# Performance work log

Measured on AMD Instinct MI355X. Metric: run time of the kernel, lower is better.

## Reference

```python
import jax, jax.numpy as jnp
import numpy as np
import math

B, S, D = 4, 1024, 1024
H, DK = 16, 64
NUM_BUCKETS = 32
MAX_DISTANCE = 128


def _relative_position_bucket(relative_position, bidirectional=True,
                              num_buckets=32, max_distance=128):
    # faithful port of T5's bucketing
    relative_buckets = jnp.zeros_like(relative_position)
    if bidirectional:
        num_buckets //= 2
        relative_buckets = relative_buckets + (relative_position > 0).astype(jnp.int32) * num_buckets
        relative_position = jnp.abs(relative_position)
    else:
        relative_position = -jnp.minimum(relative_position, jnp.zeros_like(relative_position))
    max_exact = num_buckets // 2
    is_small = relative_position < max_exact
    rp_safe = jnp.maximum(relative_position, 1)  # avoid log(0); masked by is_small
    rel_if_large = max_exact + (
        jnp.log(rp_safe.astype(jnp.float32) / max_exact)
        / math.log(max_distance / max_exact) * (num_buckets - max_exact)
    ).astype(jnp.int32)
    rel_if_large = jnp.minimum(rel_if_large, num_buckets - 1)
    return relative_buckets + jnp.where(is_small, relative_position, rel_if_large)


def compute_bias(rel_bias_emb, query_length, key_length):
    ctx = jnp.arange(query_length, dtype=jnp.int32)[:, None]
    mem = jnp.arange(key_length, dtype=jnp.int32)[None, :]
    rp = mem - ctx  # [q, k]
    buckets = _relative_position_bucket(rp, bidirectional=True,
                                        num_buckets=NUM_BUCKETS,
                                        max_distance=MAX_DISTANCE)
    values = rel_bias_emb[buckets]          # [q, k, h]
    return jnp.transpose(values, (2, 0, 1))[None]  # [1, h, q, k]


def setup_inputs() -> dict:
    key = jax.random.key(0)
    ks = jax.random.split(key, 6)
    s = 1.0 / math.sqrt(D)
    return {
        "hidden_states": jax.random.normal(ks[0], (B, S, D), jnp.float32),
        "Wq": jax.random.normal(ks[1], (D, H * DK), jnp.float32) * s,
        "Wk": jax.random.normal(ks[2], (D, H * DK), jnp.float32) * s,
        "Wv": jax.random.normal(ks[3], (D, H * DK), jnp.float32) * s,
        "Wo": jax.random.normal(ks[4], (H * DK, D), jnp.float32) * s,
        "rel_bias_emb": jax.random.normal(ks[5], (NUM_BUCKETS, H), jnp.float32),
    }


def reference(hidden_states, Wq, Wk, Wv, Wo, rel_bias_emb):
    b, s, _ = hidden_states.shape

    def shape_heads(x):  # [b, s, h*dk] -> [b, h, s, dk]
        return x.reshape(b, s, H, DK).transpose(0, 2, 1, 3)

    q = shape_heads(hidden_states @ Wq)
    k = shape_heads(hidden_states @ Wk)
    v = shape_heads(hidden_states @ Wv)

    # T5 attention: no 1/sqrt(dk) scaling
    scores = jnp.einsum('bhqd,bhkd->bhqk', q, k)
    position_bias = compute_bias(rel_bias_emb, s, s)  # [1, h, s, s]
    scores = scores + position_bias
    attn = jax.nn.softmax(scores.astype(jnp.float32), axis=-1).astype(scores.dtype)
    ctx = jnp.einsum('bhqk,bhkd->bhqd', attn, v)
    ctx = ctx.transpose(0, 2, 1, 3).reshape(b, s, H * DK)
    return ctx @ Wo
```

## Files before the change

kernel.cpp:

```cpp
#include <hip/hip_runtime.h>

typedef unsigned short u16;
typedef unsigned int u32;
typedef __bf16 bf16x8 __attribute__((ext_vector_type(8)));
typedef float f32x4 __attribute__((ext_vector_type(4)));

#define MFMA16(a, b, c) __builtin_amdgcn_mfma_f32_16x16x32_bf16(a, b, c, 0, 0, 0)
#define LOG2E 1.4426950408889634f

__device__ __forceinline__ u16 f2bf(float f) {
  u32 u = __float_as_uint(f);
  u += 0x7FFFu + ((u >> 16) & 1u);
  return (u16)(u >> 16);
}

__device__ __forceinline__ void gld16(u16* lds, const u16* g) {
  __builtin_amdgcn_global_load_lds((const __attribute__((address_space(1))) void*)g,
                                   (__attribute__((address_space(3))) void*)lds,
                                   16, 0, 0);
}

__device__ __forceinline__ int t5_bucket(int rp) {
  int ret = rp > 0 ? 16 : 0;
  int a = rp < 0 ? -rp : rp;
  int b;
  if      (a <  8) b = a;
  else if (a < 12) b = 8;
  else if (a < 16) b = 9;
  else if (a < 23) b = 10;
  else if (a < 32) b = 11;
  else if (a < 46) b = 12;
  else if (a < 64) b = 13;
  else if (a < 91) b = 14;
  else             b = 15;
  return ret + b;
}

__global__ __launch_bounds__(256) void prep(const float4* __restrict__ X, ushort4* __restrict__ Xb,
                                            const float* __restrict__ w0, const float* __restrict__ w1,
                                            const float* __restrict__ w2, const float* __restrict__ w3,
                                            u16* __restrict__ out) {
  int bid = blockIdx.x;
  if (bid < 512) {
#pragma unroll
    for (int i = 0; i < 8; i++) {
      int g = bid * 2048 + i * 256 + threadIdx.x;
      float4 v = X[g];
      ushort4 o;
      o.x = f2bf(v.x); o.y = f2bf(v.y); o.z = f2bf(v.z); o.w = f2bf(v.w);
      Xb[g] = o;
    }
    return;
  }
  bid -= 512;
  __shared__ __align__(16) u16 tb[64 * 68];
  const int col = threadIdx.x & 63;
  const int rowo = threadIdx.x >> 6;
#pragma unroll 1
  for (int t2 = 0; t2 < 2; t2++) {
    const int tile = bid * 2 + t2;
    const int z = tile >> 8, t = tile & 255;
    const float* W = (z == 0) ? w0 : (z == 1) ? w1 : (z == 2) ? w2 : w3;
    u16* O = out + z * 1048576;
    const int n0 = (t & 15) * 64, k0 = (t >> 4) * 64;
#pragma unroll
    for (int r = 0; r < 16; r++) {
      int kl = r * 4 + rowo;
      tb[col * 68 + kl] = f2bf(W[(k0 + kl) * 1024 + n0 + col]);
    }
    __syncthreads();
#pragma unroll
    for (int r = 0; r < 16; r++) {
      int nl = r * 4 + rowo;
      O[(n0 + nl) * 1024 + k0 + col] = tb[nl * 68 + col];
    }
    __syncthreads();
  }
}

__global__ __launch_bounds__(256) void gemm128(const u16* __restrict__ A,
                                               const u16* __restrict__ BtBase,
                                               u16* __restrict__ outp) {
  __shared__ __align__(16) u16 smem[18432];
  u16* sA = smem;
  u16* sB = smem + 8192;
  const int tid = threadIdx.x, lane = tid & 63, wave = tid >> 6;
  const int l15 = lane & 15, quad = lane >> 4;
  const int wm = (wave >> 1) * 64, wn = (wave & 1) * 64;

  const int id = blockIdx.x + blockIdx.y * 24;
  const int xcd = id & 7, jj = id >> 3;
  const int nz = (jj % 12) + (xcd & 1) * 12;
  const int ymb = (jj / 12) + (xcd >> 1) * 8;
  const int n = nz / 3, z = nz % 3;
  const int m0 = ymb * 128, n0 = n * 128;
  const u16* Bt = BtBase + z * 1048576;

  f32x4 acc[4][4];
  const f32x4 vz = {0.f, 0.f, 0.f, 0.f};
#pragma unroll
  for (int i = 0; i < 4; i++)
#pragma unroll
    for (int j = 0; j < 4; j++) acc[i][j] = vz;

  const int sx = l15 & 7;

  for (int kt = 0; kt < 16; kt++) {
    const int ka = kt * 64;
#pragma unroll
    for (int r = 0; r < 4; r++) {
      int cb = r * 256 + wave * 64;
      int cc = cb + lane;
      int row = cc >> 3, c8 = (cc & 7) ^ (row & 7);
      gld16(sA + cb * 8, A  + (m0 + row) * 1024 + ka + c8 * 8);
      gld16(sB + cb * 8, Bt + (n0 + row) * 1024 + ka + c8 * 8);
    }
    __syncthreads();
#pragma unroll
    for (int kk = 0; kk < 2; kk++) {
      bf16x8 af[4], bg[4];
      int g8 = kk * 4 + quad;
#pragma unroll
      for (int mt = 0; mt < 4; mt++)
        af[mt] = *(const bf16x8*)(sA + (wm + mt * 16 + l15) * 64 + (g8 ^ sx) * 8);
#pragma unroll
      for (int nt = 0; nt < 4; nt++)
        bg[nt] = *(const bf16x8*)(sB + (wn + nt * 16 + l15) * 64 + (g8 ^ sx) * 8);
#pragma unroll
      for (int mt = 0; mt < 4; mt++)
#pragma unroll
        for (int nt = 0; nt < 4; nt++)
          acc[mt][nt] = MFMA16(af[mt], bg[nt], acc[mt][nt]);
    }
    __syncthreads();
  }

  if (z == 2) {
    u16* O = outp + z * 4194304;
#pragma unroll
    for (int mt = 0; mt < 4; mt++)
#pragma unroll
      for (int nt = 0; nt < 4; nt++) {
        int col = wn + nt * 16 + l15;
        int rowb = wm + mt * 16 + quad * 4;
        uint2 p;
        p.x = (u32)f2bf(acc[mt][nt][0]) | ((u32)f2bf(acc[mt][nt][1]) << 16);
        p.y = (u32)f2bf(acc[mt][nt][2]) | ((u32)f2bf(acc[mt][nt][3]) << 16);
        *(uint2*)(smem + col * 136 + rowb) = p;
      }
    __syncthreads();
    const int b = m0 >> 10, sbase = m0 & 1023;
#pragma unroll
    for (int p = 0; p < 8; p++) {
      int g = p * 256 + tid;
      int col = g >> 4, chunk = g & 15;
      uint4 v = *(const uint4*)(smem + col * 136 + chunk * 8);
      int nn = n0 + col, hh = nn >> 6, dk = nn & 63;
      *(uint4*)(O + ((b * 16 + hh) * 64 + dk) * 1024 + sbase + chunk * 8) = v;
    }
  } else {
    u16* O = outp + z * 4194304;
    const float scl = (z == 0) ? LOG2E : 1.0f;
#pragma unroll
    for (int mt = 0; mt < 4; mt++)
#pragma unroll
      for (int nt = 0; nt < 4; nt++) {
        int rowb = wm + mt * 16 + quad * 4;
        int colb = wn + nt * 16 + l15;
#pragma unroll
        for (int reg = 0; reg < 4; reg++)
          smem[(rowb + reg) * 144 + colb] = f2bf(acc[mt][nt][reg] * scl);
      }
    __syncthreads();
    const int b = m0 >> 10, sbase = m0 & 1023;
#pragma unroll
    for (int p = 0; p < 8; p++) {
      int g = p * 256 + tid;
      int ml = g >> 4, c = g & 15;
      uint4 v = *(const uint4*)(smem + ml * 144 + c * 8);
      int nn = n0 + c * 8, hh = nn >> 6, dk = nn & 63;
      *(uint4*)(O + (b * 16 + hh) * 65536 + (sbase + ml) * 64 + dk) = v;
    }
  }
}

__global__ __launch_bounds__(256) void attn(const u16* __restrict__ Q, const u16* __restrict__ K,
                                            const u16* __restrict__ V, const float* __restrict__ emb,
                                            u16* __restrict__ ctx) {
  __shared__ __align__(16) u16 sK[64 * 64];
  __shared__ __align__(16) u16 sV[64 * 64];
  __shared__ __align__(16) u16 sP[128 * 72];
  __shared__ __align__(16) float4 bt4[1156];
  const int tid = threadIdx.x, lane = tid & 63, wave = tid >> 6;
  const int l15 = lane & 15, quad = lane >> 4;
  const int bh = blockIdx.x, qt = blockIdx.y;
  const int h = bh & 15, b = bh >> 4;
  const u16* Qp = Q + bh * 65536 + qt * 8192;
  const u16* Kp = K + bh * 65536;
  const u16* Vp = V + bh * 65536;
  const int sx = l15 & 7;

  bf16x8 aq[2][2];
#pragma unroll
  for (int u = 0; u < 2; u++)
#pragma unroll
    for (int kk = 0; kk < 2; kk++)
      aq[u][kk] = *(const bf16x8*)(Qp + (wave * 32 + u * 16 + l15) * 64 + kk * 32 + quad * 8);

  for (int i = tid; i < 1156; i += 256) {
    int rp0 = i - 127 - qt * 128;
    float4 v;
    v.x = emb[t5_bucket(rp0)     * 16 + h] * LOG2E;
    v.y = emb[t5_bucket(rp0 + 1) * 16 + h] * LOG2E;
    v.z = emb[t5_bucket(rp0 + 2) * 16 + h] * LOG2E;
    v.w = emb[t5_bucket(rp0 + 3) * 16 + h] * LOG2E;
    bt4[i] = v;
  }
  const float bias_pos = emb[31 * 16 + h] * LOG2E;
  const float bias_neg = emb[15 * 16 + h] * LOG2E;

  float2 ls2[2] = {{0.f, 0.f}, {0.f, 0.f}};
  f32x4 oc[2][4];
  const f32x4 vzero = {0.f, 0.f, 0.f, 0.f};
#pragma unroll
  for (int u = 0; u < 2; u++)
#pragma unroll
    for (int nt = 0; nt < 4; nt++) oc[u][nt] = vzero;

  __syncthreads();

#pragma unroll 1
  for (int j = 0; j < 16; j++) {
    const u16* Kj = Kp + j * 4096;
#pragma unroll
    for (int r = 0; r < 2; r++) {
      int cb = r * 256 + wave * 64;
      int cc = cb + lane;
      int row = cc >> 3, c8 = (cc & 7) ^ (row & 7);
      gld16(sK + cb * 8, Kj + row * 64 + c8 * 8);
      gld16(sV + cb * 8, Vp + row * 1024 + j * 64 + c8 * 8);
    }
    __syncthreads();

    f32x4 sc[4][2];
    const int rp_min = j * 64 - qt * 128 - 127;
    const int rp_max = j * 64 + 63 - qt * 128;
    if (rp_min >= 91) {
#pragma unroll
      for (int mt = 0; mt < 4; mt++)
#pragma unroll
        for (int u = 0; u < 2; u++) { sc[mt][u][0] = bias_pos; sc[mt][u][1] = bias_pos; sc[mt][u][2] = bias_pos; sc[mt][u][3] = bias_pos; }
    } else if (rp_max <= -91) {
#pragma unroll
      for (int mt = 0; mt < 4; mt++)
#pragma unroll
        for (int u = 0; u < 2; u++) { sc[mt][u][0] = bias_neg; sc[mt][u][1] = bias_neg; sc[mt][u][2] = bias_neg; sc[mt][u][3] = bias_neg; }
    } else {
#pragma unroll
      for (int mt = 0; mt < 4; mt++)
#pragma unroll
        for (int u = 0; u < 2; u++) {
          int idx = j * 64 + mt * 16 + quad * 4 - wave * 32 - u * 16 - l15 + 127;
          float4 bv4 = bt4[idx];
          sc[mt][u][0] = bv4.x; sc[mt][u][1] = bv4.y; sc[mt][u][2] = bv4.z; sc[mt][u][3] = bv4.w;
        }
    }
#pragma unroll
    for (int kk = 0; kk < 2; kk++) {
      bf16x8 ak[4];
      int g8 = kk * 4 + quad;
#pragma unroll
      for (int mt = 0; mt < 4; mt++)
        ak[mt] = *(const bf16x8*)(sK + (mt * 16 + l15) * 64 + (g8 ^ sx) * 8);
#pragma unroll
      for (int mt = 0; mt < 4; mt++)
#pragma unroll
        for (int u = 0; u < 2; u++)
          sc[mt][u] = MFMA16(ak[mt], aq[u][kk], sc[mt][u]);
    }

#pragma unroll
    for (int u = 0; u < 2; u++) {
      const int prow = wave * 32 + u * 16 + l15;
#pragma unroll
      for (int mt = 0; mt < 4; mt++) {
        u32 b0 = __float_as_uint(__builtin_amdgcn_exp2f(sc[mt][u][0]));
        u32 b1 = __float_as_uint(__builtin_amdgcn_exp2f(sc[mt][u][1]));
        u32 b2 = __float_as_uint(__builtin_amdgcn_exp2f(sc[mt][u][2]));
        u32 b3 = __float_as_uint(__builtin_amdgcn_exp2f(sc[mt][u][3]));
        u32 t0 = b0 & 0xFFFF0000u, t1 = b1 & 0xFFFF0000u;
        u32 t2 = b2 & 0xFFFF0000u, t3 = b3 & 0xFFFF0000u;
        ls2[u].x += __uint_as_float(t0) + __uint_as_float(t2);
        ls2[u].y += __uint_as_float(t1) + __uint_as_float(t3);
        uint2 pk;
        pk.x = (t0 >> 16) | t1;
        pk.y = (t2 >> 16) | t3;
        *(uint2*)(sP + prow * 72 + mt * 16 + quad * 4) = pk;
      }
    }
    asm volatile("s_waitcnt lgkmcnt(0)" ::: "memory");

#pragma unroll
    for (int kk = 0; kk < 2; kk++) {
      bf16x8 ap[2];
      int g8 = kk * 4 + quad;
#pragma unroll
      for (int u = 0; u < 2; u++)
        ap[u] = *(const bf16x8*)(sP + (wave * 32 + u * 16 + l15) * 72 + kk * 32 + quad * 8);
#pragma unroll
      for (int nt = 0; nt < 4; nt++) {
        bf16x8 bv = *(const bf16x8*)(sV + (nt * 16 + l15) * 64 + (g8 ^ sx) * 8);
#pragma unroll
        for (int u = 0; u < 2; u++)
          oc[u][nt] = MFMA16(ap[u], bv, oc[u][nt]);
      }
    }
    __syncthreads();
  }

  float lsum[2];
#pragma unroll
  for (int u = 0; u < 2; u++) {
    lsum[u] = ls2[u].x + ls2[u].y;
    lsum[u] += __shfl_xor(lsum[u], 16, 64);
    lsum[u] += __shfl_xor(lsum[u], 32, 64);
  }
  float linv[2][4];
#pragma unroll
  for (int u = 0; u < 2; u++)
#pragma unroll
    for (int reg = 0; reg < 4; reg++)
      linv[u][reg] = __builtin_amdgcn_rcpf(__shfl(lsum[u], quad * 4 + reg, 64));

  u16* cb2 = ctx + b * 1048576 + (qt * 128 + wave * 32) * 1024 + h * 64;
#pragma unroll
  for (int u = 0; u < 2; u++)
#pragma unroll
    for (int nt = 0; nt < 4; nt++)
#pragma unroll
      for (int reg = 0; reg < 4; reg++)
        cb2[(u * 16 + quad * 4 + reg) * 1024 + nt * 16 + l15] = f2bf(oc[u][nt][reg] * linv[u][reg]);
}

__global__ __launch_bounds__(256) void gemm_o(const u16* __restrict__ A,
                                              const u16* __restrict__ Bt,
                                              float* __restrict__ O) {
  __shared__ __align__(16) u16 sA[128 * 64];
  __shared__ __align__(16) u16 sB[64 * 64];
  const int tid = threadIdx.x, lane = tid & 63, wave = tid >> 6;
  const int l15 = lane & 15, quad = lane >> 4;
  const int wm = (wave >> 1) * 64, wn = (wave & 1) * 32;
  const int m0 = blockIdx.x * 128, n0 = blockIdx.y * 64;

  f32x4 acc[4][2];
  const f32x4 vz = {0.f, 0.f, 0.f, 0.f};
#pragma unroll
  for (int i = 0; i < 4; i++) { acc[i][0] = vz; acc[i][1] = vz; }

  const int sx = l15 & 7;

  for (int kt = 0; kt < 16; kt++) {
    const int ka = kt * 64;
#pragma unroll
    for (int r = 0; r < 4; r++) {
      int cb = r * 256 + wave * 64;
      int cc = cb + lane;
      int row = cc >> 3, c8 = (cc & 7) ^ (row & 7);
      gld16(sA + cb * 8, A + (m0 + row) * 1024 + ka + c8 * 8);
    }
#pragma unroll
    for (int r = 0; r < 2; r++) {
      int cb = r * 256 + wave * 64;
      int cc = cb + lane;
      int row = cc >> 3, c8 = (cc & 7) ^ (row & 7);
      gld16(sB + cb * 8, Bt + (n0 + row) * 1024 + ka + c8 * 8);
    }
    __syncthreads();
#pragma unroll
    for (int kk = 0; kk < 2; kk++) {
      bf16x8 af[4], bg[2];
      int g8 = kk * 4 + quad;
#pragma unroll
      for (int mt = 0; mt < 4; mt++)
        af[mt] = *(const bf16x8*)(sA + (wm + mt * 16 + l15) * 64 + (g8 ^ sx) * 8);
#pragma unroll
      for (int nt = 0; nt < 2; nt++)
        bg[nt] = *(const bf16x8*)(sB + (wn + nt * 16 + l15) * 64 + (g8 ^ sx) * 8);
#pragma unroll
      for (int mt = 0; mt < 4; mt++)
#pragma unroll
        for (int nt = 0; nt < 2; nt++)
          acc[mt][nt] = MFMA16(af[mt], bg[nt], acc[mt][nt]);
    }
    __syncthreads();
  }

#pragma unroll
  for (int mt = 0; mt < 4; mt++)
#pragma unroll
    for (int nt = 0; nt < 2; nt++)
#pragma unroll
      for (int reg = 0; reg < 4; reg++) {
        int row = m0 + wm + mt * 16 + quad * 4 + reg;
        int col = n0 + wn + nt * 16 + l15;
        O[row * 1024 + col] = acc[mt][nt][reg];
      }
}

extern "C" void kernel_launch(void* const* d_in, const int* in_sizes, int n_in,
                              void* d_out, int out_size, void* d_ws, size_t ws_size,
                              hipStream_t stream) {
  (void)in_sizes; (void)n_in; (void)out_size; (void)ws_size;
  const float* X   = (const float*)d_in[0];
  const float* Wq  = (const float*)d_in[1];
  const float* Wk  = (const float*)d_in[2];
  const float* Wv  = (const float*)d_in[3];
  const float* Wo  = (const float*)d_in[4];
  const float* emb = (const float*)d_in[5];

  char* ws = (char*)d_ws;
  u16* Xb  = (u16*)(ws);
  u16* Wt  = (u16*)(ws + (8u  << 20));
  u16* Qb  = (u16*)(ws + (16u << 20));
  u16* Ctx = (u16*)(ws + (40u << 20));

  prep<<<1024, 256, 0, stream>>>((const float4*)X, (ushort4*)Xb, Wq, Wk, Wv, Wo, Wt);
  gemm128<<<dim3(24, 32), 256, 0, stream>>>(Xb, Wt, Qb);
  attn<<<dim3(64, 8), 256, 0, stream>>>(Qb, Qb + 4194304, Qb + 2 * 4194304, emb, Ctx);
  gemm_o<<<dim3(32, 16), 256, 0, stream>>>(Ctx, Wt + 3 * 1048576, (float*)d_out);
}
```

Measured before the change: 173.2 us.

## Register-prefetch next K tile in GEMMs and enlarge output GEMM tile

Both the QKV projection GEMM and the output GEMM drop direct global-to-LDS loads. They now prefetch the next K-slice into registers while the current slice is multiplied, then write it to shared memory after the barrier. The output GEMM tile grows from 128x64 to 128x128, halving the grid and doubling per-wave MFMA work and B-tile reuse, and launch bounds are added to cap register use. The aim is to hide global load latency behind compute. The cost is higher register pressure, extra VGPR-to-LDS store instructions, and fewer blocks for the output GEMM (256 on a large GPU).

New measurement: 293.4 us. 1.69x slower.

```diff
diff --git a/kernel.cpp b/kernel.cpp
--- a/kernel.cpp
+++ b/kernel.cpp
@@ -78,9 +78,9 @@
   }
 }
 
-__global__ __launch_bounds__(256) void gemm128(const u16* __restrict__ A,
-                                               const u16* __restrict__ BtBase,
-                                               u16* __restrict__ outp) {
+__global__ __launch_bounds__(256, 3) void gemm128(const u16* __restrict__ A,
+                                                  const u16* __restrict__ BtBase,
+                                                  u16* __restrict__ outp) {
   __shared__ __align__(16) u16 smem[18432];
   u16* sA = smem;
   u16* sB = smem + 8192;
@@ -94,7 +94,17 @@
   const int ymb = (jj / 12) + (xcd >> 1) * 8;
   const int n = nz / 3, z = nz % 3;
   const int m0 = ymb * 128, n0 = n * 128;
-  const u16* Bt = BtBase + z * 1048576;
+  const u16* Ab = A + m0 * 1024;
+  const u16* Bb = BtBase + z * 1048576 + n0 * 1024;
+
+  int srow[4], soff[4], sdst[4];
+#pragma unroll
+  for (int r = 0; r < 4; r++) {
+    int cc = r * 256 + wave * 64 + lane;
+    srow[r] = cc >> 3;
+    soff[r] = srow[r] * 1024 + ((cc & 7) ^ (srow[r] & 7)) * 8;
+    sdst[r] = cc * 8;
+  }
 
   f32x4 acc[4][4];
   const f32x4 vz = {0.f, 0.f, 0.f, 0.f};
@@ -105,17 +115,29 @@
 
   const int sx = l15 & 7;
 
+  uint4 pa[4], pb[4];
+#pragma unroll
+  for (int r = 0; r < 4; r++) {
+    pa[r] = *(const uint4*)(Ab + soff[r]);
+    pb[r] = *(const uint4*)(Bb + soff[r]);
+  }
+#pragma unroll
+  for (int r = 0; r < 4; r++) {
+    *(uint4*)(sA + sdst[r]) = pa[r];
+    *(uint4*)(sB + sdst[r]) = pb[r];
+  }
+
+#pragma unroll 1
   for (int kt = 0; kt < 16; kt++) {
-    const int ka = kt * 64;
-#pragma unroll
-    for (int r = 0; r < 4; r++) {
-      int cb = r * 256 + wave * 64;
-      int cc = cb + lane;
-      int row = cc >> 3, c8 = (cc & 7) ^ (row & 7);
-      gld16(sA + cb * 8, A  + (m0 + row) * 1024 + ka + c8 * 8);
-      gld16(sB + cb * 8, Bt + (n0 + row) * 1024 + ka + c8 * 8);
-    }
-    __syncthreads();
+    __syncthreads();
+    if (kt < 15) {
+      const int ka = (kt + 1) * 64;
+#pragma unroll
+      for (int r = 0; r < 4; r++) {
+        pa[r] = *(const uint4*)(Ab + ka + soff[r]);
+        pb[r] = *(const uint4*)(Bb + ka + soff[r]);
+      }
+    }
 #pragma unroll
     for (int kk = 0; kk < 2; kk++) {
       bf16x8 af[4], bg[4];
@@ -133,6 +155,13 @@
           acc[mt][nt] = MFMA16(af[mt], bg[nt], acc[mt][nt]);
     }
     __syncthreads();
+    if (kt < 15) {
+#pragma unroll
+      for (int r = 0; r < 4; r++) {
+        *(uint4*)(sA + sdst[r]) = pa[r];
+        *(uint4*)(sB + sdst[r]) = pb[r];
+      }
+    }
   }
 
   if (z == 2) {
@@ -342,63 +371,89 @@
         cb2[(u * 16 + quad * 4 + reg) * 1024 + nt * 16 + l15] = f2bf(oc[u][nt][reg] * linv[u][reg]);
 }
 
-__global__ __launch_bounds__(256) void gemm_o(const u16* __restrict__ A,
-                                              const u16* __restrict__ Bt,
-                                              float* __restrict__ O) {
+__global__ __launch_bounds__(256, 2) void gemm_o(const u16* __restrict__ A,
+                                                 const u16* __restrict__ Bt,
+                                                 float* __restrict__ O) {
   __shared__ __align__(16) u16 sA[128 * 64];
-  __shared__ __align__(16) u16 sB[64 * 64];
+  __shared__ __align__(16) u16 sB[128 * 64];
   const int tid = threadIdx.x, lane = tid & 63, wave = tid >> 6;
   const int l15 = lane & 15, quad = lane >> 4;
-  const int wm = (wave >> 1) * 64, wn = (wave & 1) * 32;
-  const int m0 = blockIdx.x * 128, n0 = blockIdx.y * 64;
-
-  f32x4 acc[4][2];
+  const int wm = (wave >> 1) * 64, wn = (wave & 1) * 64;
+  const int m0 = blockIdx.x * 128, n0 = blockIdx.y * 128;
+  const u16* Ab = A + m0 * 1024;
+  const u16* Bb = Bt + n0 * 1024;
+
+  int srow[4], soff[4], sdst[4];
+#pragma unroll
+  for (int r = 0; r < 4; r++) {
+    int cc = r * 256 + wave * 64 + lane;
+    srow[r] = cc >> 3;
+    soff[r] = srow[r] * 1024 + ((cc & 7) ^ (srow[r] & 7)) * 8;
+    sdst[r] = cc * 8;
+  }
+
+  f32x4 acc[4][4];
   const f32x4 vz = {0.f, 0.f, 0.f, 0.f};
 #pragma unroll
-  for (int i = 0; i < 4; i++) { acc[i][0] = vz; acc[i][1] = vz; }
+  for (int i = 0; i < 4; i++)
+#pragma unroll
+    for (int j = 0; j < 4; j++) acc[i][j] = vz;
 
   const int sx = l15 & 7;
 
+  uint4 pa[4], pb[4];
+#pragma unroll
+  for (int r = 0; r < 4; r++) {
+    pa[r] = *(const uint4*)(Ab + soff[r]);
+    pb[r] = *(const uint4*)(Bb + soff[r]);
+  }
+#pragma unroll
+  for (int r = 0; r < 4; r++) {
+    *(uint4*)(sA + sdst[r]) = pa[r];
+    *(uint4*)(sB + sdst[r]) = pb[r];
+  }
+
+#pragma unroll 1
   for (int kt = 0; kt < 16; kt++) {
-    const int ka = kt * 64;
-#pragma unroll
-    for (int r = 0; r < 4; r++) {
-      int cb = r * 256 + wave * 64;
-      int cc = cb + lane;
-      int row = cc >> 3, c8 = (cc & 7) ^ (row & 7);
-      gld16(sA + cb * 8, A + (m0 + row) * 1024 + ka + c8 * 8);
-    }
-#pragma unroll
-    for (int r = 0; r < 2; r++) {
-      int cb = r * 256 + wave * 64;
-      int cc = cb + lane;
-      int row = cc >> 3, c8 = (cc & 7) ^ (row & 7);
-      gld16(sB + cb * 8, Bt + (n0 + row) * 1024 + ka + c8 * 8);
-    }
-    __syncthreads();
+    __syncthreads();
+    if (kt < 15) {
+      const int ka = (kt + 1) * 64;
+#pragma unroll
+      for (int r = 0; r < 4; r++) {
+        pa[r] = *(const uint4*)(Ab + ka + soff[r]);
+        pb[r] = *(const uint4*)(Bb + ka + soff[r]);
+      }
+    }
 #pragma unroll
     for (int kk = 0; kk < 2; kk++) {
-      bf16x8 af[4], bg[2];
+      bf16x8 af[4], bg[4];
       int g8 = kk * 4 + quad;
 #pragma unroll
       for (int mt = 0; mt < 4; mt++)
         af[mt] = *(const bf16x8*)(sA + (wm + mt * 16 + l15) * 64 + (g8 ^ sx) * 8);
 #pragma unroll
-      for (int nt = 0; nt < 2; nt++)
+      for (int nt = 0; nt < 4; nt++)
         bg[nt] = *(const bf16x8*)(sB + (wn + nt * 16 + l15) * 64 + (g8 ^ sx) * 8);
 #pragma unroll
       for (int mt = 0; mt < 4; mt++)
 #pragma unroll
-        for (int nt = 0; nt < 2; nt++)
+        for (int nt = 0; nt < 4; nt++)
           acc[mt][nt] = MFMA16(af[mt], bg[nt], acc[mt][nt]);
     }
     __syncthreads();
+    if (kt < 15) {
+#pragma unroll
+      for (int r = 0; r < 4; r++) {
+        *(uint4*)(sA + sdst[r]) = pa[r];
+        *(uint4*)(sB + sdst[r]) = pb[r];
+      }
+    }
   }
 
 #pragma unroll
   for (int mt = 0; mt < 4; mt++)
 #pragma unroll
-    for (int nt = 0; nt < 2; nt++)
+    for (int nt = 0; nt < 4; nt++)
 #pragma unroll
       for (int reg = 0; reg < 4; reg++) {
         int row = m0 + wm + mt * 16 + quad * 4 + reg;
@@ -427,5 +482,5 @@
   prep<<<1024, 256, 0, stream>>>((const float4*)X, (ushort4*)Xb, Wq, Wk, Wv, Wo, Wt);
   gemm128<<<dim3(24, 32), 256, 0, stream>>>(Xb, Wt, Qb);
   attn<<<dim3(64, 8), 256, 0, stream>>>(Qb, Qb + 4194304, Qb + 2 * 4194304, emb, Ctx);
-  gemm_o<<<dim3(32, 16), 256, 0, stream>>>(Ctx, Wt + 3 * 1048576, (float*)d_out);
-}
+  gemm_o<<<dim3(32, 8), 256, 0, stream>>>(Ctx, Wt + 3 * 1048576, (float*)d_out);
+}
```

## Double-buffer LDS loads in QKV and output GEMMs with async prefetch

Applied to the files above, without the earlier changes.

Both GEMM kernels now use two LDS buffers. The next k-tile's global_load_lds is issued before computing on the current one, and the waits are manual vmcnt/s_barrier instead of full __syncthreads, so memory latency overlaps with MFMA work. The QKV GEMM switches to 32-wide k-tiles with a new XOR swizzle so the double buffer fits in the same LDS. The output GEMM changes its tile shape to 64x128 with four waves along N, and its grid changes to match. The trade-offs are more LDS per block and a hand-counted vmcnt that must match the number of loads in flight.

Result: faster. 164.8 us (-4.8%).

```diff
diff --git a/kernel.cpp b/kernel.cpp
--- a/kernel.cpp
+++ b/kernel.cpp
@@ -82,8 +82,6 @@
                                                const u16* __restrict__ BtBase,
                                                u16* __restrict__ outp) {
   __shared__ __align__(16) u16 smem[18432];
-  u16* sA = smem;
-  u16* sB = smem + 8192;
   const int tid = threadIdx.x, lane = tid & 63, wave = tid >> 6;
   const int l15 = lane & 15, quad = lane >> 4;
   const int wm = (wave >> 1) * 64, wn = (wave & 1) * 64;
@@ -94,7 +92,13 @@
   const int ymb = (jj / 12) + (xcd >> 1) * 8;
   const int n = nz / 3, z = nz % 3;
   const int m0 = ymb * 128, n0 = n * 128;
-  const u16* Bt = BtBase + z * 1048576;
+  const u16* Ab = A + m0 * 1024;
+  const u16* Bb = BtBase + z * 1048576 + n0 * 1024;
+
+  int cc0 = tid, cc1 = 256 + tid;
+  int row0 = cc0 >> 2, row1 = cc1 >> 2;
+  int aoff0 = row0 * 1024 + (((cc0 & 3) ^ ((row0 >> 1) & 3)) * 8);
+  int aoff1 = row1 * 1024 + (((cc1 & 3) ^ ((row1 >> 1) & 3)) * 8);
 
   f32x4 acc[4][4];
   const f32x4 vz = {0.f, 0.f, 0.f, 0.f};
@@ -103,37 +107,45 @@
 #pragma unroll
     for (int j = 0; j < 4; j++) acc[i][j] = vz;
 
-  const int sx = l15 & 7;
-
-  for (int kt = 0; kt < 16; kt++) {
-    const int ka = kt * 64;
-#pragma unroll
-    for (int r = 0; r < 4; r++) {
-      int cb = r * 256 + wave * 64;
-      int cc = cb + lane;
-      int row = cc >> 3, c8 = (cc & 7) ^ (row & 7);
-      gld16(sA + cb * 8, A  + (m0 + row) * 1024 + ka + c8 * 8);
-      gld16(sB + cb * 8, Bt + (n0 + row) * 1024 + ka + c8 * 8);
-    }
-    __syncthreads();
-#pragma unroll
-    for (int kk = 0; kk < 2; kk++) {
-      bf16x8 af[4], bg[4];
-      int g8 = kk * 4 + quad;
-#pragma unroll
-      for (int mt = 0; mt < 4; mt++)
-        af[mt] = *(const bf16x8*)(sA + (wm + mt * 16 + l15) * 64 + (g8 ^ sx) * 8);
+  const int sk = (l15 >> 1) & 3;
+
+  {
+    u16* st = smem;
+    gld16(st + cc0 * 8, Ab + aoff0);
+    gld16(st + cc1 * 8, Ab + aoff1);
+    gld16(st + 4096 + cc0 * 8, Bb + aoff0);
+    gld16(st + 4096 + cc1 * 8, Bb + aoff1);
+  }
+
+#pragma unroll 1
+  for (int kt = 0; kt < 32; kt++) {
+    u16* st = smem + (kt & 1) * 8192;
+    if (kt < 31) {
+      u16* dst = smem + ((kt + 1) & 1) * 8192;
+      const int ka = (kt + 1) * 32;
+      gld16(dst + cc0 * 8, Ab + ka + aoff0);
+      gld16(dst + cc1 * 8, Ab + ka + aoff1);
+      gld16(dst + 4096 + cc0 * 8, Bb + ka + aoff0);
+      gld16(dst + 4096 + cc1 * 8, Bb + ka + aoff1);
+      asm volatile("s_waitcnt vmcnt(4)\n\ts_barrier" ::: "memory");
+    } else {
+      asm volatile("s_waitcnt vmcnt(0)\n\ts_barrier" ::: "memory");
+    }
+    bf16x8 af[4], bg[4];
+#pragma unroll
+    for (int mt = 0; mt < 4; mt++)
+      af[mt] = *(const bf16x8*)(st + (wm + mt * 16 + l15) * 32 + ((quad ^ sk) * 8));
+#pragma unroll
+    for (int nt = 0; nt < 4; nt++)
+      bg[nt] = *(const bf16x8*)(st + 4096 + (wn + nt * 16 + l15) * 32 + ((quad ^ sk) * 8));
+#pragma unroll
+    for (int mt = 0; mt < 4; mt++)
 #pragma unroll
       for (int nt = 0; nt < 4; nt++)
-        bg[nt] = *(const bf16x8*)(sB + (wn + nt * 16 + l15) * 64 + (g8 ^ sx) * 8);
-#pragma unroll
-      for (int mt = 0; mt < 4; mt++)
-#pragma unroll
-        for (int nt = 0; nt < 4; nt++)
-          acc[mt][nt] = MFMA16(af[mt], bg[nt], acc[mt][nt]);
-    }
-    __syncthreads();
-  }
+        acc[mt][nt] = MFMA16(af[mt], bg[nt], acc[mt][nt]);
+    asm volatile("s_barrier" ::: "memory");
+  }
+  __syncthreads();
 
   if (z == 2) {
     u16* O = outp + z * 4194304;
@@ -345,12 +357,26 @@
 __global__ __launch_bounds__(256) void gemm_o(const u16* __restrict__ A,
                                               const u16* __restrict__ Bt,
                                               float* __restrict__ O) {
-  __shared__ __align__(16) u16 sA[128 * 64];
-  __shared__ __align__(16) u16 sB[64 * 64];
+  __shared__ __align__(16) u16 smem[24576];
   const int tid = threadIdx.x, lane = tid & 63, wave = tid >> 6;
   const int l15 = lane & 15, quad = lane >> 4;
-  const int wm = (wave >> 1) * 64, wn = (wave & 1) * 32;
-  const int m0 = blockIdx.x * 128, n0 = blockIdx.y * 64;
+  const int m0 = blockIdx.x * 64, n0 = blockIdx.y * 128;
+  const u16* Ab = A + m0 * 1024;
+  const u16* Bb = Bt + n0 * 1024;
+  const int wn = wave * 32;
+
+  int ac = tid, bc0 = tid, bc1 = 256 + tid, bc2 = 512 + tid, bc3 = 768 + tid;
+  int ar0 = tid >> 3, ar1 = (256 + tid) >> 3;
+  int aoff0 = ar0 * 1024 + (((tid & 7) ^ (ar0 & 7)) * 8);
+  int aoff1 = ar1 * 1024 + ((((256 + tid) & 7) ^ (ar1 & 7)) * 8);
+  int boff[4], bdst[4];
+#pragma unroll
+  for (int r = 0; r < 4; r++) {
+    int cc = r * 256 + tid;
+    int row = cc >> 3;
+    boff[r] = row * 1024 + (((cc & 7) ^ (row & 7)) * 8);
+    bdst[r] = cc * 8;
+  }
 
   f32x4 acc[4][2];
   const f32x4 vz = {0.f, 0.f, 0.f, 0.f};
@@ -359,40 +385,45 @@
 
   const int sx = l15 & 7;
 
+  {
+    u16* st = smem;
+    gld16(st + tid * 8, Ab + aoff0);
+    gld16(st + (256 + tid) * 8, Ab + aoff1);
+#pragma unroll
+    for (int r = 0; r < 4; r++) gld16(st + 4096 + bdst[r], Bb + boff[r]);
+  }
+
+#pragma unroll 1
   for (int kt = 0; kt < 16; kt++) {
-    const int ka = kt * 64;
-#pragma unroll
-    for (int r = 0; r < 4; r++) {
-      int cb = r * 256 + wave * 64;
-      int cc = cb + lane;
-      int row = cc >> 3, c8 = (cc & 7) ^ (row & 7);
-      gld16(sA + cb * 8, A + (m0 + row) * 1024 + ka + c8 * 8);
-    }
-#pragma unroll
-    for (int r = 0; r < 2; r++) {
-      int cb = r * 256 + wave * 64;
-      int cc = cb + lane;
-      int row = cc >> 3, c8 = (cc & 7) ^ (row & 7);
-      gld16(sB + cb * 8, Bt + (n0 + row) * 1024 + ka + c8 * 8);
-    }
-    __syncthreads();
+    u16* st = smem + (kt & 1) * 12288;
+    if (kt < 15) {
+      u16* dst = smem + ((kt + 1) & 1) * 12288;
+      const int ka = (kt + 1) * 64;
+      gld16(dst + tid * 8, Ab + ka + aoff0);
+      gld16(dst + (256 + tid) * 8, Ab + ka + aoff1);
+#pragma unroll
+      for (int r = 0; r < 4; r++) gld16(dst + 4096 + bdst[r], Bb + ka + boff[r]);
+      asm volatile("s_waitcnt vmcnt(6)\n\ts_barrier" ::: "memory");
+    } else {
+      asm volatile("s_waitcnt vmcnt(0)\n\ts_barrier" ::: "memory");
+    }
 #pragma unroll
     for (int kk = 0; kk < 2; kk++) {
       bf16x8 af[4], bg[2];
       int g8 = kk * 4 + quad;
 #pragma unroll
       for (int mt = 0; mt < 4; mt++)
-        af[mt] = *(const bf16x8*)(sA + (wm + mt * 16 + l15) * 64 + (g8 ^ sx) * 8);
+        af[mt] = *(const bf16x8*)(st + (mt * 16 + l15) * 64 + ((g8 ^ sx) * 8));
 #pragma unroll
       for (int nt = 0; nt < 2; nt++)
-        bg[nt] = *(const bf16x8*)(sB + (wn + nt * 16 + l15) * 64 + (g8 ^ sx) * 8);
+        bg[nt] = *(const bf16x8*)(st + 4096 + (wn + nt * 16 + l15) * 64 + ((g8 ^ sx) * 8));
 #pragma unroll
       for (int mt = 0; mt < 4; mt++)
 #pragma unroll
         for (int nt = 0; nt < 2; nt++)
           acc[mt][nt] = MFMA16(af[mt], bg[nt], acc[mt][nt]);
     }
-    __syncthreads();
+    asm volatile("s_barrier" ::: "memory");
   }
 
 #pragma unroll
@@ -401,7 +432,7 @@
     for (int nt = 0; nt < 2; nt++)
 #pragma unroll
       for (int reg = 0; reg < 4; reg++) {
-        int row = m0 + wm + mt * 16 + quad * 4 + reg;
+        int row = m0 + mt * 16 + quad * 4 + reg;
         int col = n0 + wn + nt * 16 + l15;
         O[row * 1024 + col] = acc[mt][nt][reg];
       }
@@ -427,5 +458,5 @@
   prep<<<1024, 256, 0, stream>>>((const float4*)X, (ushort4*)Xb, Wq, Wk, Wv, Wo, Wt);
   gemm128<<<dim3(24, 32), 256, 0, stream>>>(Xb, Wt, Qb);
   attn<<<dim3(64, 8), 256, 0, stream>>>(Qb, Qb + 4194304, Qb + 2 * 4194304, emb, Ctx);
-  gemm_o<<<dim3(32, 16), 256, 0, stream>>>(Ctx, Wt + 3 * 1048576, (float*)d_out);
-}
+  gemm_o<<<dim3(64, 8), 256, 0, stream>>>(Ctx, Wt + 3 * 1048576, (float*)d_out);
+}
```
